# Optimization experiments

Measured on AMD Instinct MI355X. Metric: run time of the kernel, lower is better.

Reference implementation:

```python
import jax, jax.numpy as jnp
from jax import lax
import numpy as np

B, T, H, IN = 256, 1024, 256, 1

def setup_inputs() -> dict:
    key = jax.random.key(0)
    ks = jax.random.split(key, 9)
    s = 1.0 / np.sqrt(H)  # PyTorch default uniform(-1/sqrt(H), 1/sqrt(H)); use scaled normal
    return {
        "x": jax.random.normal(ks[0], (B, T, IN), jnp.float32),
        "W_ih0": jax.random.normal(ks[1], (4 * H, IN), jnp.float32) * s,
        "W_hh0": jax.random.normal(ks[2], (4 * H, H), jnp.float32) * s,
        "b_ih0": jax.random.normal(ks[3], (4 * H,), jnp.float32) * s,
        "b_hh0": jax.random.normal(ks[4], (4 * H,), jnp.float32) * s,
        "W_ih1": jax.random.normal(ks[5], (4 * H, H), jnp.float32) * s,
        "W_hh1": jax.random.normal(ks[6], (4 * H, H), jnp.float32) * s,
        "b_ih1": jax.random.normal(ks[7], (4 * H,), jnp.float32) * s,
        "b_hh1": jax.random.normal(ks[8], (4 * H,), jnp.float32) * s,
    }

def _lstm_layer(x, W_ih, W_hh, b_ih, b_hh):
    # x: [B, T, D_in] -> (y [B, T, H], h_T [B, H], c_T [B, H]); gates ordered i,f,g,o (PyTorch)
    b, t = x.shape[0], x.shape[1]
    h = W_hh.shape[1]
    # precompute input projection for all timesteps: [T, B, 4H]
    xp = jnp.swapaxes(jnp.einsum('btd,gd->btg', x, W_ih) + b_ih + b_hh, 0, 1)

    def step(carry, xt):
        hprev, cprev = carry
        gates = xt + hprev @ W_hh.T  # [B, 4H]
        i, f, g, o = jnp.split(gates, 4, axis=-1)
        i = jax.nn.sigmoid(i)
        f = jax.nn.sigmoid(f)
        g = jnp.tanh(g)
        o = jax.nn.sigmoid(o)
        c = f * cprev + i * g
        hnew = o * jnp.tanh(c)
        return (hnew, c), hnew

    h0 = jnp.zeros((b, h), x.dtype)
    (hT, cT), ys = lax.scan(step, (h0, h0), xp)
    return jnp.swapaxes(ys, 0, 1), hT, cT

def reference(x, W_ih0, W_hh0, b_ih0, b_hh0, W_ih1, W_hh1, b_ih1, b_hh1):
    y0, h0, c0 = _lstm_layer(x, W_ih0, W_hh0, b_ih0, b_hh0)
    # inter-layer dropout(0.1) is train-only; inference = identity
    _, h1, c1 = _lstm_layer(y0, W_ih1, W_hh1, b_ih1, b_hh1)
    h_n = jnp.stack([h0, h1], axis=0)  # [num_layers, B, H]
    c_n = jnp.stack([c0, c1], axis=0)
    return h_n, c_n
```

## Files before the change

### kernel.cpp

```cpp
#include <hip/hip_runtime.h>


#define TSTEPS 1024u

typedef __attribute__((ext_vector_type(8))) short bf16x8;
typedef __attribute__((ext_vector_type(4))) float f32x4;

__device__ __forceinline__ unsigned short f2bf(float f) {
  unsigned u = __float_as_uint(f);
  u += 0x7FFFu + ((u >> 16) & 1u);
  return (unsigned short)(u >> 16);
}
__device__ __forceinline__ float sigm(float x) { return 1.0f / (1.0f + __expf(-x)); }
__device__ __forceinline__ float tanh_f(float x) {
  float xc = fminf(fmaxf(x, -15.0f), 15.0f);
  float e = __expf(2.0f * xc);
  return (e - 1.0f) / (e + 1.0f);
}

__global__ __launch_bounds__(256, 1) void lstm2_v6(
    const float* __restrict__ x,
    const float* __restrict__ Wih0,
    const float* __restrict__ Whh0,
    const float* __restrict__ bih0, const float* __restrict__ bhh0,
    const float* __restrict__ Wih1,
    const float* __restrict__ Whh1,
    const float* __restrict__ bih1, const float* __restrict__ bhh1,
    float* __restrict__ out,
    unsigned long long* __restrict__ fastb,
    unsigned long long* __restrict__ slowb,
    unsigned* __restrict__ ctrl)
{
  const int bid  = blockIdx.x;
  const int c    = bid & 15;
  const int iw   = bid >> 4;
  const int tid  = threadIdx.x;
  const int lane = tid & 63;
  const int wv   = tid >> 6;
  const int hi   = lane >> 4;
  const int lm   = lane & 15;

  const unsigned long long TB = 0x4000400040004000ULL;

  unsigned myxcc;
  asm volatile("s_getreg_b32 %0, hwreg(HW_REG_XCC_ID)" : "=s"(myxcc));
  myxcc &= 0xFu;
  if (tid == 0)
    __hip_atomic_store(&ctrl[bid], 0x5A5A0000u | myxcc,
                       __ATOMIC_RELAXED, __HIP_MEMORY_SCOPE_AGENT);

  bf16x8 w0[8], wi1[8], wh1[8];
  {
    const int wrow = (lm & 3) * 256 + (iw << 4) + (wv << 2) + (lm >> 2);
    const int kb   = hi << 3;
#pragma unroll
    for (int kk = 0; kk < 8; ++kk) {
      const int k0 = kk * 32 + kb;
      const float* p0 = Whh0 + (size_t)wrow * 256 + k0;
      const float* p1 = Wih1 + (size_t)wrow * 256 + k0;
      const float* p2 = Whh1 + (size_t)wrow * 256 + k0;
      bf16x8 a, b, cc;
#pragma unroll
      for (int e = 0; e < 8; ++e) {
        a[e]  = (short)f2bf(p0[e]);
        b[e]  = (short)f2bf(p1[e]);
        cc[e] = (short)f2bf(p2[e]);
      }
      w0[kk] = a; wi1[kk] = b; wh1[kk] = cc;
    }
  }

  const int rowE = lm;
  const int jg   = (iw << 4) + (wv << 2) + hi;
  float wx[4], bs0[4], bs1[4];
#pragma unroll
  for (int r = 0; r < 4; ++r) {
    const int col = (r << 8) + jg;
    wx[r]  = Wih0[col];
    bs0[r] = bih0[col] + bhh0[col];
    bs1[r] = bih1[col] + bhh1[col];
  }

  unsigned ofs_[8], lofs_[8];
#pragma unroll
  for (int i = 0; i < 8; ++i) {
    const int n   = tid + 256 * i;
    const int L   = n >> 10;
    const int row = (n >> 6) & 15;
    const int q   = n & 63;
    ofs_[i]  = (unsigned)(((c * 2 + L) * 16 + row) * 64 + q);
    lofs_[i] = (unsigned)(L * 4224 + row * 264 + q * 4);
  }

  __shared__ unsigned s_uni;
  if (tid == 0) {
    if (iw == 0) {
      unsigned x0 = 0, uni = 1u;
      for (int k = 0; k < 16 && uni; ++k) {
        unsigned v; int g2 = 0;
        for (;;) {
          v = __hip_atomic_load(&ctrl[c + 16 * k], __ATOMIC_RELAXED, __HIP_MEMORY_SCOPE_AGENT);
          if ((v & 0xFFFF0000u) == 0x5A5A0000u) break;
          if (++g2 > (1 << 15)) { uni = 0u; break; }
        }
        if (uni) {
          const unsigned xc = v & 0xFFFFu;
          if (k == 0) x0 = xc; else if (xc != x0) uni = 0u;
        }
      }
      __hip_atomic_store(&ctrl[256 + c], 0x5A5A0000u | uni,
                         __ATOMIC_RELAXED, __HIP_MEMORY_SCOPE_AGENT);
    }
    unsigned uni = 0u; int g2 = 0;
    for (;;) {
      unsigned v = __hip_atomic_load(&ctrl[256 + c], __ATOMIC_RELAXED, __HIP_MEMORY_SCOPE_AGENT);
      if ((v & 0xFFFF0000u) == 0x5A5A0000u) { uni = v & 1u; break; }
      if (++g2 > (1 << 15)) break;
    }
    s_uni = uni;
  }
  __syncthreads();
  const bool uniform = (s_uni != 0u);
  unsigned long long* pollb = uniform ? fastb : slowb;

  __shared__ __align__(16) unsigned short A[2 * 2 * 16 * 264];

  const float* xrow = x + (size_t)((c << 4) + rowE) * TSTEPS;
  float4 xq = {0.f, 0.f, 0.f, 0.f};

  float c0 = 0.f, h0f = 0.f, c1 = 0.f, h1f = 0.f;
  bool dead = false;

  for (unsigned s = 0; s <= TSTEPS; ++s) {
    if ((s & 3u) == 0u && s < TSTEPS) xq = *(const float4*)(xrow + s);
    const float xv = (s & 2u) ? ((s & 1u) ? xq.w : xq.z) : ((s & 1u) ? xq.y : xq.x);

    const unsigned t4 = s & 15u;
    const unsigned long long em =
        ((unsigned long long)(t4 & 1u)        << 14) |
        ((unsigned long long)((t4 >> 1) & 1u) << 30) |
        ((unsigned long long)((t4 >> 2) & 1u) << 46) |
        ((unsigned long long)((t4 >> 3) & 1u) << 62);
    const unsigned tau = s + 1u;
    const unsigned long long emn =
        ((unsigned long long)(tau & 1u)        << 14) |
        ((unsigned long long)((tau >> 1) & 1u) << 30) |
        ((unsigned long long)((tau >> 2) & 1u) << 46) |
        ((unsigned long long)((tau >> 3) & 1u) << 62);
    unsigned long long* fb = fastb + (size_t)(tau & 1u) * 32768u;
    unsigned long long* sb = slowb + (size_t)(tau & 1u) * 32768u;
    const unsigned long long* pb = pollb + (size_t)(s & 1u) * 32768u;
    unsigned short* Ap = A + (s & 1u) * 8448u;

    if (s == 0) {
      for (int z = tid; z < 8448; z += 256) ((unsigned*)A)[z] = 0u;
    } else {
      unsigned long long vv[8];
      int guard = 0;
      while (!dead) {
#pragma unroll
        for (int i = 0; i < 8; ++i)
          vv[i] = __hip_atomic_load(pb + ofs_[i], __ATOMIC_RELAXED, __HIP_MEMORY_SCOPE_AGENT);
        bool ok = true;
#pragma unroll
        for (int i = 0; i < 8; ++i) ok &= ((vv[i] & TB) == em);
        if (__all(ok)) break;
        if (++guard > (1 << 14)) dead = true;
      }
#pragma unroll
      for (int i = 0; i < 8; ++i)
        *(unsigned long long*)&Ap[lofs_[i]] = vv[i] & ~TB;
    }
    __syncthreads();

    bf16x8 af0[8];
    f32x4 acc0a = {0.f, 0.f, 0.f, 0.f}, acc0b = {0.f, 0.f, 0.f, 0.f};
    const unsigned short* a0p = Ap + lm * 264 + (hi << 3);
    const unsigned short* a1p = a0p + 4224;
#pragma unroll
    for (int kk = 0; kk < 4; ++kk) {
      af0[kk] = *(const bf16x8*)(a0p + kk * 32);
      acc0a = __builtin_amdgcn_mfma_f32_16x16x32_bf16(w0[kk], af0[kk], acc0a, 0, 0, 0);
    }
#pragma unroll
    for (int kk = 4; kk < 8; ++kk) {
      af0[kk] = *(const bf16x8*)(a0p + kk * 32);
      acc0b = __builtin_amdgcn_mfma_f32_16x16x32_bf16(w0[kk], af0[kk], acc0b, 0, 0, 0);
    }

    f32x4 a1a0 = {0.f, 0.f, 0.f, 0.f}, a1a1 = {0.f, 0.f, 0.f, 0.f};
    f32x4 a1b0 = {0.f, 0.f, 0.f, 0.f}, a1b1 = {0.f, 0.f, 0.f, 0.f};
#pragma unroll
    for (int kk = 0; kk < 4; ++kk) {
      a1a0 = __builtin_amdgcn_mfma_f32_16x16x32_bf16(wi1[kk], af0[kk], a1a0, 0, 0, 0);
      const bf16x8 a1f = *(const bf16x8*)(a1p + kk * 32);
      a1b0 = __builtin_amdgcn_mfma_f32_16x16x32_bf16(wh1[kk], a1f, a1b0, 0, 0, 0);
    }
#pragma unroll
    for (int kk = 4; kk < 8; ++kk) {
      a1a1 = __builtin_amdgcn_mfma_f32_16x16x32_bf16(wi1[kk], af0[kk], a1a1, 0, 0, 0);
      const bf16x8 a1f = *(const bf16x8*)(a1p + kk * 32);
      a1b1 = __builtin_amdgcn_mfma_f32_16x16x32_bf16(wh1[kk], a1f, a1b1, 0, 0, 0);
    }

    if (s < TSTEPS) {
      const float pi = (acc0a[0] + acc0b[0]) + xv * wx[0] + bs0[0];
      const float pf = (acc0a[1] + acc0b[1]) + xv * wx[1] + bs0[1];
      const float pg = (acc0a[2] + acc0b[2]) + xv * wx[2] + bs0[2];
      const float po = (acc0a[3] + acc0b[3]) + xv * wx[3] + bs0[3];
      const float ig = sigm(pi), fg = sigm(pf), gv = tanh_f(pg), og = sigm(po);
      c0  = fg * c0 + ig * gv;
      h0f = og * tanh_f(c0);

      const int v   = (int)(unsigned)f2bf(h0f);
      const int p16 = __shfl_xor(v, 16);
      const unsigned part = (unsigned)(unsigned short)v | ((unsigned)(unsigned short)p16 << 16);
      const unsigned p32  = (unsigned)__shfl_xor((int)part, 32);
      unsigned long long v64 = (unsigned long long)part | ((unsigned long long)p32 << 32);
      v64 = (v64 & ~TB) | emn;
      const unsigned i0 = ((c * 2 + 0) * 16 + (unsigned)rowE) * 64 + (unsigned)((iw << 2) + wv);
      if (hi == 0) {
        __hip_atomic_store(fb + i0, v64, __ATOMIC_RELAXED, __HIP_MEMORY_SCOPE_WORKGROUP);
        if (!uniform)
          __hip_atomic_store(sb + i0, v64, __ATOMIC_RELAXED, __HIP_MEMORY_SCOPE_AGENT);
      }
    }

    if (s >= 1u) {
      const float pi = (a1a0[0] + a1a1[0]) + (a1b0[0] + a1b1[0]) + bs1[0];
      const float pf = (a1a0[1] + a1a1[1]) + (a1b0[1] + a1b1[1]) + bs1[1];
      const float pg = (a1a0[2] + a1a1[2]) + (a1b0[2] + a1b1[2]) + bs1[2];
      const float po = (a1a0[3] + a1a1[3]) + (a1b0[3] + a1b1[3]) + bs1[3];
      const float ig = sigm(pi), fg = sigm(pf), gv = tanh_f(pg), og = sigm(po);
      c1  = fg * c1 + ig * gv;
      h1f = og * tanh_f(c1);
    }
    if (s < TSTEPS) {
      const int v   = (int)(unsigned)f2bf(h1f);
      const int p16 = __shfl_xor(v, 16);
      const unsigned part = (unsigned)(unsigned short)v | ((unsigned)(unsigned short)p16 << 16);
      const unsigned p32  = (unsigned)__shfl_xor((int)part, 32);
      unsigned long long v64 = (unsigned long long)part | ((unsigned long long)p32 << 32);
      v64 = (v64 & ~TB) | emn;
      const unsigned i1 = ((c * 2 + 1) * 16 + (unsigned)rowE) * 64 + (unsigned)((iw << 2) + wv);
      if (hi == 0) {
        __hip_atomic_store(fb + i1, v64, __ATOMIC_RELAXED, __HIP_MEMORY_SCOPE_WORKGROUP);
        if (!uniform)
          __hip_atomic_store(sb + i1, v64, __ATOMIC_RELAXED, __HIP_MEMORY_SCOPE_AGENT);
      }
    }
  }

  {
    const int b  = (c << 4) + rowE;
    const size_t o = (size_t)b * 256 + jg;
    out[o]                  = h0f;
    out[65536 + o]          = h1f;
    out[131072 + o]         = c0;
    out[131072 + 65536 + o] = c1;
  }
}

extern "C" void kernel_launch(void* const* d_in, const int* in_sizes, int n_in,
                              void* d_out, int out_size, void* d_ws, size_t ws_size,
                              hipStream_t stream) {
  const float* x    = (const float*)d_in[0];
  const float* Wih0 = (const float*)d_in[1];
  const float* Whh0 = (const float*)d_in[2];
  const float* bih0 = (const float*)d_in[3];
  const float* bhh0 = (const float*)d_in[4];
  const float* Wih1 = (const float*)d_in[5];
  const float* Whh1 = (const float*)d_in[6];
  const float* bih1 = (const float*)d_in[7];
  const float* bhh1 = (const float*)d_in[8];

  unsigned long long* fastb = (unsigned long long*)d_ws;
  unsigned long long* slowb;
  unsigned* ctrl;
  if (ws_size >= (1u << 20) + 2048u) {
    slowb = fastb + 65536;
    ctrl  = (unsigned*)(fastb + 131072);
  } else {
    slowb = fastb;
    ctrl  = (unsigned*)((char*)d_ws + (512u << 10));
  }

  lstm2_v6<<<256, 256, 0, stream>>>(x, Wih0, Whh0, bih0, bhh0,
                                    Wih1, Whh1, bih1, bhh1,
                                    (float*)d_out, fastb, slowb, ctrl);
}
```

Before: 1.812 ms.

## Replace in-band tag-bit polling with per-wave step flags for inter-block sync

Each wave stopped embedding step tag bits in the bf16 payload and polling every data word for them. It now writes its data, waits on vmcnt, then publishes a per-wave step counter flag. Consumers poll a single 64-entry flag row per cluster and load the payload only once all flags show the step. This shrinks the polled footprint and removes the tag masking, but adds an extra store and a waitcnt on the critical path. Correctness relies on the ordering between the data stores and the relaxed flag store, plus a shorter dead-guard timeout.

```diff
diff --git a/kernel.cpp b/kernel.cpp
--- a/kernel.cpp
+++ b/kernel.cpp
@@ -2,6 +2,7 @@
 
 
 #define TSTEPS 1024u
+#define FMAGIC 0x5A5A0000u
 
 typedef __attribute__((ext_vector_type(8))) short bf16x8;
 typedef __attribute__((ext_vector_type(4))) float f32x4;
@@ -18,7 +19,7 @@
   return (e - 1.0f) / (e + 1.0f);
 }
 
-__global__ __launch_bounds__(256, 1) void lstm2_v6(
+__global__ __launch_bounds__(256, 1) void lstm2_v7(
     const float* __restrict__ x,
     const float* __restrict__ Wih0,
     const float* __restrict__ Whh0,
@@ -29,7 +30,9 @@
     float* __restrict__ out,
     unsigned long long* __restrict__ fastb,
     unsigned long long* __restrict__ slowb,
-    unsigned* __restrict__ ctrl)
+    unsigned* __restrict__ ctrl,
+    unsigned* __restrict__ flagF,
+    unsigned* __restrict__ flagS)
 {
   const int bid  = blockIdx.x;
   const int c    = bid & 15;
@@ -40,13 +43,11 @@
   const int hi   = lane >> 4;
   const int lm   = lane & 15;
 
-  const unsigned long long TB = 0x4000400040004000ULL;
-
   unsigned myxcc;
   asm volatile("s_getreg_b32 %0, hwreg(HW_REG_XCC_ID)" : "=s"(myxcc));
   myxcc &= 0xFu;
   if (tid == 0)
-    __hip_atomic_store(&ctrl[bid], 0x5A5A0000u | myxcc,
+    __hip_atomic_store(&ctrl[bid], FMAGIC | myxcc,
                        __ATOMIC_RELAXED, __HIP_MEMORY_SCOPE_AGENT);
 
   bf16x8 w0[8], wi1[8], wh1[8];
@@ -100,7 +101,7 @@
         unsigned v; int g2 = 0;
         for (;;) {
           v = __hip_atomic_load(&ctrl[c + 16 * k], __ATOMIC_RELAXED, __HIP_MEMORY_SCOPE_AGENT);
-          if ((v & 0xFFFF0000u) == 0x5A5A0000u) break;
+          if ((v & 0xFFFF0000u) == FMAGIC) break;
           if (++g2 > (1 << 15)) { uni = 0u; break; }
         }
         if (uni) {
@@ -108,20 +109,24 @@
           if (k == 0) x0 = xc; else if (xc != x0) uni = 0u;
         }
       }
-      __hip_atomic_store(&ctrl[256 + c], 0x5A5A0000u | uni,
+      __hip_atomic_store(&ctrl[256 + c], FMAGIC | uni,
                          __ATOMIC_RELAXED, __HIP_MEMORY_SCOPE_AGENT);
     }
     unsigned uni = 0u; int g2 = 0;
     for (;;) {
       unsigned v = __hip_atomic_load(&ctrl[256 + c], __ATOMIC_RELAXED, __HIP_MEMORY_SCOPE_AGENT);
-      if ((v & 0xFFFF0000u) == 0x5A5A0000u) { uni = v & 1u; break; }
+      if ((v & 0xFFFF0000u) == FMAGIC) { uni = v & 1u; break; }
       if (++g2 > (1 << 15)) break;
     }
     s_uni = uni;
   }
   __syncthreads();
   const bool uniform = (s_uni != 0u);
-  unsigned long long* pollb = uniform ? fastb : slowb;
+  unsigned long long* pollD = uniform ? fastb : slowb;
+  unsigned*           pollF = uniform ? flagF : flagS;
+  unsigned*           myFlagF = &flagF[(c << 6) + (iw << 2) + wv];
+  unsigned*           myFlagS = &flagS[(c << 6) + (iw << 2) + wv];
+  unsigned*           fl      = pollF + (c << 6);
 
   __shared__ __align__(16) unsigned short A[2 * 2 * 16 * 264];
 
@@ -135,41 +140,28 @@
     if ((s & 3u) == 0u && s < TSTEPS) xq = *(const float4*)(xrow + s);
     const float xv = (s & 2u) ? ((s & 1u) ? xq.w : xq.z) : ((s & 1u) ? xq.y : xq.x);
 
-    const unsigned t4 = s & 15u;
-    const unsigned long long em =
-        ((unsigned long long)(t4 & 1u)        << 14) |
-        ((unsigned long long)((t4 >> 1) & 1u) << 30) |
-        ((unsigned long long)((t4 >> 2) & 1u) << 46) |
-        ((unsigned long long)((t4 >> 3) & 1u) << 62);
-    const unsigned tau = s + 1u;
-    const unsigned long long emn =
-        ((unsigned long long)(tau & 1u)        << 14) |
-        ((unsigned long long)((tau >> 1) & 1u) << 30) |
-        ((unsigned long long)((tau >> 2) & 1u) << 46) |
-        ((unsigned long long)((tau >> 3) & 1u) << 62);
-    unsigned long long* fb = fastb + (size_t)(tau & 1u) * 32768u;
-    unsigned long long* sb = slowb + (size_t)(tau & 1u) * 32768u;
-    const unsigned long long* pb = pollb + (size_t)(s & 1u) * 32768u;
+    unsigned long long* fb = fastb + (size_t)((s + 1u) & 1u) * 32768u;
+    unsigned long long* sb = slowb + (size_t)((s + 1u) & 1u) * 32768u;
+    const unsigned long long* pb = pollD + (size_t)(s & 1u) * 32768u;
     unsigned short* Ap = A + (s & 1u) * 8448u;
 
     if (s == 0) {
       for (int z = tid; z < 8448; z += 256) ((unsigned*)A)[z] = 0u;
     } else {
-      unsigned long long vv[8];
+      const unsigned want = FMAGIC + s;
       int guard = 0;
       while (!dead) {
-#pragma unroll
-        for (int i = 0; i < 8; ++i)
-          vv[i] = __hip_atomic_load(pb + ofs_[i], __ATOMIC_RELAXED, __HIP_MEMORY_SCOPE_AGENT);
-        bool ok = true;
-#pragma unroll
-        for (int i = 0; i < 8; ++i) ok &= ((vv[i] & TB) == em);
-        if (__all(ok)) break;
-        if (++guard > (1 << 14)) dead = true;
-      }
+        const unsigned f = __hip_atomic_load(fl + lane, __ATOMIC_RELAXED, __HIP_MEMORY_SCOPE_AGENT);
+        if (__all((int)((f - want) < 0x10000u))) break;
+        if (++guard > (1 << 12)) dead = true;
+      }
+      unsigned long long vv[8];
 #pragma unroll
       for (int i = 0; i < 8; ++i)
-        *(unsigned long long*)&Ap[lofs_[i]] = vv[i] & ~TB;
+        vv[i] = __hip_atomic_load(pb + ofs_[i], __ATOMIC_RELAXED, __HIP_MEMORY_SCOPE_AGENT);
+#pragma unroll
+      for (int i = 0; i < 8; ++i)
+        *(unsigned long long*)&Ap[lofs_[i]] = vv[i];
     }
     __syncthreads();
 
@@ -216,8 +208,7 @@
       const int p16 = __shfl_xor(v, 16);
       const unsigned part = (unsigned)(unsigned short)v | ((unsigned)(unsigned short)p16 << 16);
       const unsigned p32  = (unsigned)__shfl_xor((int)part, 32);
-      unsigned long long v64 = (unsigned long long)part | ((unsigned long long)p32 << 32);
-      v64 = (v64 & ~TB) | emn;
+      const unsigned long long v64 = (unsigned long long)part | ((unsigned long long)p32 << 32);
       const unsigned i0 = ((c * 2 + 0) * 16 + (unsigned)rowE) * 64 + (unsigned)((iw << 2) + wv);
       if (hi == 0) {
         __hip_atomic_store(fb + i0, v64, __ATOMIC_RELAXED, __HIP_MEMORY_SCOPE_WORKGROUP);
@@ -240,13 +231,21 @@
       const int p16 = __shfl_xor(v, 16);
       const unsigned part = (unsigned)(unsigned short)v | ((unsigned)(unsigned short)p16 << 16);
       const unsigned p32  = (unsigned)__shfl_xor((int)part, 32);
-      unsigned long long v64 = (unsigned long long)part | ((unsigned long long)p32 << 32);
-      v64 = (v64 & ~TB) | emn;
+      const unsigned long long v64 = (unsigned long long)part | ((unsigned long long)p32 << 32);
       const unsigned i1 = ((c * 2 + 1) * 16 + (unsigned)rowE) * 64 + (unsigned)((iw << 2) + wv);
       if (hi == 0) {
         __hip_atomic_store(fb + i1, v64, __ATOMIC_RELAXED, __HIP_MEMORY_SCOPE_WORKGROUP);
         if (!uniform)
           __hip_atomic_store(sb + i1, v64, __ATOMIC_RELAXED, __HIP_MEMORY_SCOPE_AGENT);
+      }
+
+      asm volatile("s_waitcnt vmcnt(0)" ::: "memory");
+      if (lane == 0) {
+        const unsigned fv = FMAGIC + s + 1u;
+        if (uniform)
+          __hip_atomic_store(myFlagF, fv, __ATOMIC_RELAXED, __HIP_MEMORY_SCOPE_WORKGROUP);
+        else
+          __hip_atomic_store(myFlagS, fv, __ATOMIC_RELAXED, __HIP_MEMORY_SCOPE_AGENT);
       }
     }
   }
@@ -276,16 +275,20 @@
 
   unsigned long long* fastb = (unsigned long long*)d_ws;
   unsigned long long* slowb;
-  unsigned* ctrl;
-  if (ws_size >= (1u << 20) + 2048u) {
+  unsigned *ctrl, *flagF, *flagS;
+  if (ws_size >= (1u << 20) + 12288u) {
     slowb = fastb + 65536;
     ctrl  = (unsigned*)(fastb + 131072);
+    flagF = ctrl + 512;
+    flagS = flagF + 1024;
   } else {
     slowb = fastb;
     ctrl  = (unsigned*)((char*)d_ws + (512u << 10));
-  }
-
-  lstm2_v6<<<256, 256, 0, stream>>>(x, Wih0, Whh0, bih0, bhh0,
+    flagF = ctrl + 512;
+    flagS = flagF;
+  }
+
+  lstm2_v7<<<256, 256, 0, stream>>>(x, Wih0, Whh0, bih0, bhh0,
                                     Wih1, Whh1, bih1, bhh1,
-                                    (float*)d_out, fastb, slowb, ctrl);
-}
+                                    (float*)d_out, fastb, slowb, ctrl, flagF, flagS);
+}
```

Result: no change. 1.807 ms (-0.3%).
